# Optimization experiments

Measured on AMD Instinct MI355X. Metric: run time of the kernel, lower is better.

## Reference

```python
import jax, jax.numpy as jnp
import numpy as np
from jax import lax
from jax.scipy.special import logsumexp

XY, Z, V, WS = 16, 8, 10000, 2
S = XY * XY * Z            # 2048 states
EMB, TOK, HID = 256, 100, 256
B, T, L = 8, 16, 12
EPS = 1e-5


def residual(x, w1, b1, w2, b2, g, beta):
    # ResidualLayer: relu(lin1) -> relu(lin2) -> LayerNorm(x2 + x1)
    x1 = jax.nn.relu(x @ w1.T + b1)
    x2 = jax.nn.relu(x1 @ w2.T + b2)
    h = x2 + x1
    mu = h.mean(-1, keepdims=True)
    var = ((h - mu) ** 2).mean(-1, keepdims=True)
    return (h - mu) * lax.rsqrt(var + EPS) * g + beta


def win_logmean(m, axis, ws):
    win = 2 * ws + 1
    pads = [(0, 0)] * m.ndim
    pads[axis] = (ws, ws)
    p = jnp.pad(m, pads, mode='edge')
    d = m.shape[axis]
    acc = lax.dynamic_slice_in_dim(p, 0, d, axis)
    for k in range(1, win):
        acc = jnp.logaddexp(acc, lax.dynamic_slice_in_dim(p, k, d, axis))
    return acc - jnp.log(jnp.float32(win))


def setup_inputs() -> dict:
    key = jax.random.key(0)
    it = iter(jax.random.split(key, 64))

    def rn(shape, scale=0.05):
        return jax.random.normal(next(it), shape, jnp.float32) * scale

    inp = {}
    inp['state_emb'] = jax.random.normal(next(it), (S, EMB), jnp.float32)
    inp['tok_emb'] = jax.random.normal(next(it), (V, TOK), jnp.float32)

    def res(pfx, din, dout):
        inp[pfx + '_w1'] = rn((dout, din))
        inp[pfx + '_b1'] = jnp.zeros((dout,), jnp.float32)
        inp[pfx + '_w2'] = rn((dout, dout))
        inp[pfx + '_b2'] = jnp.zeros((dout,), jnp.float32)
        inp[pfx + '_g'] = jnp.ones((dout,), jnp.float32)
        inp[pfx + '_beta'] = jnp.zeros((dout,), jnp.float32)

    res('start', EMB, HID)
    inp['start_wo'] = rn((1, HID))
    inp['start_bo'] = jnp.zeros((1,), jnp.float32)
    res('tin', EMB, HID)
    res('tout', EMB, HID)
    res('emit', EMB, TOK)
    inp['stories'] = jax.random.randint(next(it), (B, T, L), 0, V + 1)  # id V = pad
    inp['story_length'] = T
    return inp


def reference(state_emb, tok_emb,
              start_w1, start_b1, start_w2, start_b2, start_g, start_beta, start_wo, start_bo,
              tin_w1, tin_b1, tin_w2, tin_b2, tin_g, tin_beta,
              tout_w1, tout_b1, tout_w2, tout_b2, tout_g, tout_beta,
              emit_w1, emit_b1, emit_w2, emit_b2, emit_g, emit_beta,
              stories, story_length):
    # prior_log_p: [S]
    h0 = residual(state_emb, start_w1, start_b1, start_w2, start_b2, start_g, start_beta)
    priors = jax.nn.log_softmax((h0 @ start_wo.T + start_bo)[:, 0], axis=-1)

    # transition_log_p: sparse-neighbor masked [S,S] log-softmax
    h_in = residual(state_emb, tin_w1, tin_b1, tin_w2, tin_b2, tin_g, tin_beta)
    h_out = residual(state_emb, tout_w1, tout_b1, tout_w2, tout_b2, tout_g, tout_beta)
    trans = h_in @ h_out.T
    idx = jnp.arange(S)
    offs = jnp.array([0, 1, -1, XY, -XY, XY * XY, 2 * XY * XY])
    neigh = idx[:, None] + offs[None, :]                        # [S,7]
    allowed = (neigh[:, :, None] == idx[None, None, :]).any(1)  # allowed[j,i]
    trans = jax.nn.log_softmax(jnp.where(allowed, trans, -jnp.inf), axis=-1)

    # emission matrix with windowed log-mean pooling over x,y
    h_emit = residual(state_emb, emit_w1, emit_b1, emit_w2, emit_b2, emit_g, emit_beta)
    em = jax.nn.log_softmax(h_emit @ tok_emb.T, axis=1)         # [S,V]
    em = em.reshape(Z, XY, XY, V)
    em = win_logmean(em, 2, WS)   # dim -2
    em = win_logmean(em, 1, WS)   # dim -3
    em = em.reshape(S, V)
    em_pad = jnp.concatenate([em, jnp.zeros((S, 1), em.dtype)], axis=1)  # pad token
    emis = em_pad.T[stories].sum(2)                             # [B,T,S]

    # HMM forward recursion in log domain
    score0 = emis[:, 0] + priors[None, :]

    def step(score, em_t):
        new = em_t + logsumexp(trans[None, :, :] + score[:, None, :], axis=-1)
        return new, new

    _, rest = lax.scan(step, score0, jnp.moveaxis(emis[:, 1:story_length], 1, 0))
    return jnp.concatenate([score0[None], rest], axis=0)        # [T,B,S]
```

## Files before the change

kernel.cpp:

```cpp
#include <hip/hip_runtime.h>
#include <hip/hip_bf16.h>
#include <math.h>


typedef __bf16 bf16_t;
typedef __bf16 bf16x8 __attribute__((ext_vector_type(8)));
typedef float  floatx4 __attribute__((ext_vector_type(4)));
typedef short  short8  __attribute__((ext_vector_type(8)));

#define S_TOT 2048
#define NT2 79
#define LSE_LD 80
#define VPAD 10112

__global__ __launch_bounds__(256) void tokconv_k(const float* __restrict__ src,
                                                 bf16_t* __restrict__ dst) {
    int idx = blockIdx.x * 256 + threadIdx.x;
    int r = idx >> 7, c = idx & 127;
    float v = (r < 10000 && c < 100) ? src[r * 100 + c] : 0.f;
    dst[idx] = (bf16_t)v;
}

struct GJob {
    const float*  Af;
    const bf16_t* Ab;
    int lda;
    const float* B; int ldb;
    int N, Nrows, K, Kvalid;
    float* C; int ldc;
    const float* bias; int nbias;
    const float* addm; int ldadd;
    bf16_t* Cbf; int ldcb;
};
struct GJobs { GJob j[4]; };

#define BM 64
#define BN 64
#define LDT 72

template<int EPI, int A32>
__global__ __launch_bounds__(256) void gemm_k(GJobs jobs) {
    GJob jb = jobs.j[blockIdx.z];
    const int m0 = blockIdx.x * BM;
    const int n0 = blockIdx.y * BN;
    if (n0 >= jb.N) return;

    __shared__ alignas(16) bf16_t As[BM * LDT];
    __shared__ alignas(16) bf16_t Bs[BN * LDT];
    const int tid  = threadIdx.x;
    const int lane = tid & 63, wave = tid >> 6;
    const int wm = (wave & 1) * 32, wn = (wave >> 1) * 32;
    const int sr = tid >> 2, scc = (tid & 3) * 16;
    const int qm = lane & 15, qk = (lane >> 4) * 8;

    floatx4 acc[2][2];
    floatx4 zf = {0.f, 0.f, 0.f, 0.f};
#pragma unroll
    for (int i = 0; i < 2; i++)
#pragma unroll
        for (int j = 0; j < 2; j++) acc[i][j] = zf;

    const bool brv = (n0 + sr) < jb.Nrows;

    for (int k0 = 0; k0 < jb.K; k0 += 64) {
        if constexpr (A32) {
            const float* Ar = jb.Af + (size_t)(m0 + sr) * jb.lda + k0 + scc;
            alignas(16) bf16_t ta[16];
#pragma unroll
            for (int i = 0; i < 4; i++) {
                float4 f = ((const float4*)Ar)[i];
                ta[i * 4 + 0] = (bf16_t)f.x; ta[i * 4 + 1] = (bf16_t)f.y;
                ta[i * 4 + 2] = (bf16_t)f.z; ta[i * 4 + 3] = (bf16_t)f.w;
            }
            *(short8*)&As[sr * LDT + scc]     = *(short8*)&ta[0];
            *(short8*)&As[sr * LDT + scc + 8] = *(short8*)&ta[8];
        } else {
            const bf16_t* Ar = jb.Ab + (size_t)(m0 + sr) * jb.lda + k0 + scc;
            *(short8*)&As[sr * LDT + scc]     = *(const short8*)&Ar[0];
            *(short8*)&As[sr * LDT + scc + 8] = *(const short8*)&Ar[8];
        }
        {
            const float* Br = jb.B + (size_t)(n0 + sr) * jb.ldb + k0 + scc;
            alignas(16) bf16_t tb[16];
#pragma unroll
            for (int i = 0; i < 4; i++) {
                int c4 = k0 + scc + i * 4;
                float4 f = {0.f, 0.f, 0.f, 0.f};
                if (brv && c4 < jb.Kvalid) f = *(const float4*)&Br[i * 4];
                tb[i * 4 + 0] = (bf16_t)f.x; tb[i * 4 + 1] = (bf16_t)f.y;
                tb[i * 4 + 2] = (bf16_t)f.z; tb[i * 4 + 3] = (bf16_t)f.w;
            }
            *(short8*)&Bs[sr * LDT + scc]     = *(short8*)&tb[0];
            *(short8*)&Bs[sr * LDT + scc + 8] = *(short8*)&tb[8];
        }
        __syncthreads();
#pragma unroll
        for (int kk = 0; kk < 2; kk++) {
            int qo = kk * 32 + qk;
            bf16x8 a[2], b[2];
            a[0] = *(const bf16x8*)&As[(wm + qm) * LDT + qo];
            a[1] = *(const bf16x8*)&As[(wm + 16 + qm) * LDT + qo];
            b[0] = *(const bf16x8*)&Bs[(wn + qm) * LDT + qo];
            b[1] = *(const bf16x8*)&Bs[(wn + 16 + qm) * LDT + qo];
#pragma unroll
            for (int mi = 0; mi < 2; mi++)
#pragma unroll
                for (int ni = 0; ni < 2; ni++)
                    acc[mi][ni] = __builtin_amdgcn_mfma_f32_16x16x32_bf16(a[mi], b[ni], acc[mi][ni], 0, 0, 0);
        }
        __syncthreads();
    }

    const int cl = lane & 15, rq = (lane >> 4) * 4;
#pragma unroll
    for (int mi = 0; mi < 2; mi++)
#pragma unroll
        for (int ni = 0; ni < 2; ni++)
#pragma unroll
            for (int r = 0; r < 4; r++) {
                int gm = m0 + wm + mi * 16 + rq + r;
                int gn = n0 + wn + ni * 16 + cl;
                if (gn < jb.N) {
                    float bv = (gn < jb.nbias) ? jb.bias[gn] : 0.f;
                    float v = fmaxf(acc[mi][ni][r] + bv, 0.f);
                    if constexpr (EPI == 1) {
                        jb.C[(size_t)gm * jb.ldc + gn] = v;
                        jb.Cbf[(size_t)gm * jb.ldcb + gn] = (bf16_t)v;
                    } else {
                        jb.C[(size_t)gm * jb.ldc + gn] = v + jb.addm[(size_t)gm * jb.ldadd + gn];
                    }
                }
            }
}

struct LJob {
    const float* h; int ld, dout;
    const float* g; const float* beta;
    float* of32; int ldo;
    bf16_t* obf; int ldob; int padN;
    const float* wo; const float* bo; float* praw;
};
struct LJobs { LJob j[4]; };

__global__ __launch_bounds__(256) void ln_k(LJobs jobs) {
    LJob jb = jobs.j[blockIdx.y];
    __shared__ float red[256];
    int row = blockIdx.x, t = threadIdx.x;
    float hv = (t < jb.dout) ? jb.h[(size_t)row * jb.ld + t] : 0.f;
    red[t] = hv;
    __syncthreads();
#pragma unroll
    for (int s = 128; s > 0; s >>= 1) { if (t < s) red[t] += red[t + s]; __syncthreads(); }
    float mu = red[0] / jb.dout;
    __syncthreads();
    float d = (t < jb.dout) ? (hv - mu) : 0.f;
    red[t] = d * d;
    __syncthreads();
#pragma unroll
    for (int s = 128; s > 0; s >>= 1) { if (t < s) red[t] += red[t + s]; __syncthreads(); }
    float var = red[0] / jb.dout;
    float rstd = rsqrtf(var + 1e-5f);
    float y = 0.f;
    if (t < jb.dout) {
        y = d * rstd * jb.g[t] + jb.beta[t];
        if (jb.of32) jb.of32[(size_t)row * jb.ldo + t] = y;
        if (jb.obf)  jb.obf[(size_t)row * jb.ldob + t] = (bf16_t)y;
    } else if (jb.obf && t < jb.padN) {
        jb.obf[(size_t)row * jb.ldob + t] = (bf16_t)0.f;
    }
    if (jb.wo) {
        __syncthreads();
        red[t] = (t < jb.dout) ? y * jb.wo[t] : 0.f;
        __syncthreads();
#pragma unroll
        for (int s = 128; s > 0; s >>= 1) { if (t < s) red[t] += red[t + s]; __syncthreads(); }
        if (t == 0) jb.praw[row] = red[0] + jb.bo[0];
    }
}

__global__ __launch_bounds__(256) void trans_k(const float* __restrict__ hin,
                                               const float* __restrict__ hout,
                                               float* __restrict__ tr,
                                               const float* __restrict__ praw,
                                               float* __restrict__ plse)
{
    __shared__ float red[256];
    if (blockIdx.x == 512) {
        int t = threadIdx.x;
        float v[8];
        float m = -INFINITY;
#pragma unroll
        for (int i = 0; i < 8; i++) { v[i] = praw[t * 8 + i]; m = fmaxf(m, v[i]); }
        red[t] = m;
        __syncthreads();
#pragma unroll
        for (int s = 128; s > 0; s >>= 1) { if (t < s) red[t] = fmaxf(red[t], red[t + s]); __syncthreads(); }
        float M = red[0];
        __syncthreads();
        float ss = 0.f;
#pragma unroll
        for (int i = 0; i < 8; i++) ss += __expf(v[i] - M);
        red[t] = ss;
        __syncthreads();
#pragma unroll
        for (int s = 128; s > 0; s >>= 1) { if (t < s) red[t] += red[t + s]; __syncthreads(); }
        if (t == 0) plse[0] = M + __logf(red[0]);
        return;
    }
    const int OFFS[7] = {0, 1, -1, 16, -16, 256, 512};
    int j = blockIdx.x * 4 + (threadIdx.x >> 6);
    int lane = threadIdx.x & 63;
    float4 a = ((const float4*)(hin + (size_t)j * 256))[lane];
    float d[7];
#pragma unroll
    for (int k = 0; k < 7; k++) {
        int i = j + OFFS[k];
        float pdot = 0.f;
        if ((unsigned)i < 2048u) {
            float4 b = ((const float4*)(hout + (size_t)i * 256))[lane];
            pdot = a.x * b.x + a.y * b.y + a.z * b.z + a.w * b.w;
        }
#pragma unroll
        for (int o = 32; o > 0; o >>= 1) pdot += __shfl_down(pdot, o);
        d[k] = pdot;
    }
    if (lane == 0) {
        float m = -INFINITY;
#pragma unroll
        for (int k = 0; k < 7; k++) { int i = j + OFFS[k]; if ((unsigned)i < 2048u) m = fmaxf(m, d[k]); }
        float ss = 0.f;
#pragma unroll
        for (int k = 0; k < 7; k++) { int i = j + OFFS[k]; if ((unsigned)i < 2048u) ss += __expf(d[k] - m); }
        float l = __logf(ss);
#pragma unroll
        for (int k = 0; k < 7; k++) {
            int i = j + OFFS[k];
            tr[(size_t)j * 8 + k] = ((unsigned)i < 2048u) ? (d[k] - m - l) : -INFINITY;
        }
        tr[(size_t)j * 8 + 7] = -INFINITY;
    }
}

__global__ __launch_bounds__(256) void lse_gemm_k(
    const bf16_t* __restrict__ hemit, const bf16_t* __restrict__ tok_bf,
    float* __restrict__ Pmax, float* __restrict__ Psum)
{
    __shared__ float pmS[2][128];
    __shared__ float psS[2][128];
    const int mb = blockIdx.x * 128;
    const int n0 = blockIdx.y * 128;
    const int tid  = threadIdx.x;
    const int lane = tid & 63, wave = tid >> 6;
    const int wm = (wave & 1) * 64, wn = (wave >> 1) * 64;
    const int qm = lane & 15, q = lane >> 4;

    floatx4 acc[4][4];
    floatx4 zf = {0.f, 0.f, 0.f, 0.f};
#pragma unroll
    for (int i = 0; i < 4; i++)
#pragma unroll
        for (int j = 0; j < 4; j++) acc[i][j] = zf;

    const bf16_t* Aw = hemit  + (size_t)(mb + wm + qm) * 128 + q * 8;
    const bf16_t* Bw = tok_bf + (size_t)(n0 + wn + qm) * 128 + q * 8;

#pragma unroll
    for (int kk = 0; kk < 4; kk++) {
        bf16x8 a[4], b[4];
#pragma unroll
        for (int i = 0; i < 4; i++) a[i] = *(const bf16x8*)&Aw[(size_t)(i * 16) * 128 + kk * 32];
#pragma unroll
        for (int i = 0; i < 4; i++) b[i] = *(const bf16x8*)&Bw[(size_t)(i * 16) * 128 + kk * 32];
#pragma unroll
        for (int mi = 0; mi < 4; mi++)
#pragma unroll
            for (int ni = 0; ni < 4; ni++)
                acc[mi][ni] = __builtin_amdgcn_mfma_f32_16x16x32_bf16(a[mi], b[ni], acc[mi][ni], 0, 0, 0);
    }

    const int cl = lane & 15, rq = (lane >> 4) * 4;
    const int half = wn >> 6;
#pragma unroll
    for (int mi = 0; mi < 4; mi++) {
#pragma unroll
        for (int r = 0; r < 4; r++) {
            float mm = -INFINITY;
#pragma unroll
            for (int ni = 0; ni < 4; ni++) {
                int gcol = n0 + wn + ni * 16 + cl;
                if (gcol < 10000) mm = fmaxf(mm, acc[mi][ni][r]);
            }
            mm = fmaxf(mm, __shfl_xor(mm, 1));
            mm = fmaxf(mm, __shfl_xor(mm, 2));
            mm = fmaxf(mm, __shfl_xor(mm, 4));
            mm = fmaxf(mm, __shfl_xor(mm, 8));
            float ss = 0.f;
#pragma unroll
            for (int ni = 0; ni < 4; ni++) {
                int gcol = n0 + wn + ni * 16 + cl;
                if (gcol < 10000) ss += __expf(acc[mi][ni][r] - mm);
            }
            ss += __shfl_xor(ss, 1);
            ss += __shfl_xor(ss, 2);
            ss += __shfl_xor(ss, 4);
            ss += __shfl_xor(ss, 8);
            if (cl == 0) {
                int row = wm + mi * 16 + rq + r;
                pmS[half][row] = mm;
                psS[half][row] = ss;
            }
        }
    }
    __syncthreads();
    if (tid < 128) {
        float ma = pmS[0][tid], mb2 = pmS[1][tid];
        float M = fmaxf(ma, mb2);
        float S = psS[0][tid] * __expf(ma - M) + psS[1][tid] * __expf(mb2 - M);
        Pmax[(size_t)(mb + tid) * LSE_LD + blockIdx.y] = M;
        Psum[(size_t)(mb + tid) * LSE_LD + blockIdx.y] = S;
    }
}

__global__ __launch_bounds__(256) void lse_fin_k(const float* __restrict__ Pmax,
                                                 const float* __restrict__ Psum,
                                                 float* __restrict__ lse)
{
    int s = (blockIdx.x * 256 + threadIdx.x) >> 6;
    int lane = threadIdx.x & 63;
    const float* pm = Pmax + (size_t)s * LSE_LD;
    const float* ps = Psum + (size_t)s * LSE_LD;
    float pv[2], sv[2];
    float m = -INFINITY;
#pragma unroll
    for (int i = 0; i < 2; i++) {
        int nb = i * 64 + lane;
        bool ok = nb < NT2;
        pv[i] = ok ? pm[nb] : -INFINITY;
        sv[i] = ok ? ps[nb] : 0.f;
        m = fmaxf(m, pv[i]);
    }
#pragma unroll
    for (int o = 1; o < 64; o <<= 1) m = fmaxf(m, __shfl_xor(m, o));
    float ss = 0.f;
#pragma unroll
    for (int i = 0; i < 2; i++) if (sv[i] > 0.f) ss += sv[i] * __expf(pv[i] - m);
#pragma unroll
    for (int o = 1; o < 64; o <<= 1) ss += __shfl_xor(ss, o);
    if (lane == 0) lse[s] = m + __logf(ss);
}

#define ELDT 136
__global__ __launch_bounds__(256) void empool_k(
    const float* __restrict__ tok_emb, const int* __restrict__ stories,
    const bf16_t* __restrict__ hemit, const float* __restrict__ lse,
    float* __restrict__ emis)
{
    __shared__ alignas(16) bf16_t As[16 * ELDT];
    __shared__ float Cs[16][260];
    __shared__ float sm2[256];
    __shared__ int stok[12];
    const int bt = blockIdx.x, z = blockIdx.y, t = threadIdx.x;
    if (t < 12) stok[t] = stories[bt * 12 + t];
    __syncthreads();
    {
        int row = t >> 4, c0 = (t & 15) * 8;
        int tok = (row < 12) ? stok[row] : 10000;
        const float* src = tok_emb + (size_t)tok * 100;
#pragma unroll
        for (int c = 0; c < 8; c++) {
            int cc = c0 + c;
            float v = (tok < 10000 && cc < 100) ? src[cc] : 0.f;
            As[row * ELDT + cc] = (bf16_t)v;
        }
    }
    __syncthreads();

    const int lane = t & 63, wave = t >> 6;
    const int qm = lane & 15, q = lane >> 4;
    floatx4 acc[4];
    floatx4 zf = {0.f, 0.f, 0.f, 0.f};
#pragma unroll
    for (int j = 0; j < 4; j++) acc[j] = zf;

#pragma unroll
    for (int kk = 0; kk < 4; kk++) {
        bf16x8 a = *(const bf16x8*)&As[qm * ELDT + kk * 32 + q * 8];
#pragma unroll
        for (int j = 0; j < 4; j++) {
            int nrow = z * 256 + (wave * 4 + j) * 16 + qm;
            bf16x8 b = *(const bf16x8*)&hemit[(size_t)nrow * 128 + kk * 32 + q * 8];
            acc[j] = __builtin_amdgcn_mfma_f32_16x16x32_bf16(a, b, acc[j], 0, 0, 0);
        }
    }
    {
        const int cl = lane & 15, rq = (lane >> 4) * 4;
#pragma unroll
        for (int j = 0; j < 4; j++) {
            int n = (wave * 4 + j) * 16 + cl;
            float ls = lse[z * 256 + n];
#pragma unroll
            for (int r = 0; r < 4; r++)
                Cs[rq + r][n] = acc[j][r] - ls;
        }
    }
    __syncthreads();

    const int a = t >> 4, b = t & 15;
    float accum = 0.f;
    for (int l = 0; l < 12; l++) {
        float m = -INFINITY;
#pragma unroll
        for (int d = -2; d <= 2; d++) {
            int bb = b + d; bb = bb < 0 ? 0 : (bb > 15 ? 15 : bb);
            m = fmaxf(m, Cs[l][a * 16 + bb]);
        }
        float ss = 0.f;
#pragma unroll
        for (int d = -2; d <= 2; d++) {
            int bb = b + d; bb = bb < 0 ? 0 : (bb > 15 ? 15 : bb);
            ss += __expf(Cs[l][a * 16 + bb] - m);
        }
        sm2[t] = m + __logf(ss);
        __syncthreads();
        float m2 = -INFINITY;
#pragma unroll
        for (int d = -2; d <= 2; d++) {
            int aa = a + d; aa = aa < 0 ? 0 : (aa > 15 ? 15 : aa);
            m2 = fmaxf(m2, sm2[aa * 16 + b]);
        }
        float s2 = 0.f;
#pragma unroll
        for (int d = -2; d <= 2; d++) {
            int aa = a + d; aa = aa < 0 ? 0 : (aa > 15 ? 15 : aa);
            s2 += __expf(sm2[aa * 16 + b] - m2);
        }
        if (stok[l] < 10000) accum += m2 + __logf(s2) - 3.2188758248682006f;
        __syncthreads();
    }
    emis[(size_t)bt * S_TOT + (size_t)z * 256 + t] = accum;
}

__global__ __launch_bounds__(1024) void fwd_k(const float* __restrict__ emm,
                                              const float* __restrict__ praw,
                                              const float* __restrict__ plse,
                                              const float* __restrict__ tr,
                                              float* __restrict__ out)
{
    const int OFFS[7] = {0, 1, -1, 16, -16, 256, 512};
    __shared__ float sc[2][S_TOT];
    int b = blockIdx.x, t = threadIdx.x;
    float pl = plse[0];
    const float* eb = emm + (size_t)b * 16 * S_TOT;

    float e[2][16];
#pragma unroll
    for (int i = 0; i < 2; i++) {
        int j = i * 1024 + t;
#pragma unroll
        for (int tt = 0; tt < 16; tt++) e[i][tt] = eb[tt * S_TOT + j];
    }
    float trj[2][7];
#pragma unroll
    for (int i = 0; i < 2; i++) {
        int j = i * 1024 + t;
        float4 lo = ((const float4*)(tr + (size_t)j * 8))[0];
        float4 hi = ((const float4*)(tr + (size_t)j * 8))[1];
        trj[i][0] = lo.x; trj[i][1] = lo.y; trj[i][2] = lo.z; trj[i][3] = lo.w;
        trj[i][4] = hi.x; trj[i][5] = hi.y; trj[i][6] = hi.z;
    }
#pragma unroll
    for (int i = 0; i < 2; i++) {
        int j = i * 1024 + t;
        float v = e[i][0] + praw[j] - pl;
        sc[0][j] = v;
        out[(size_t)b * S_TOT + j] = v;
    }
    __syncthreads();
#pragma unroll
    for (int tt = 1; tt < 16; tt++) {
        int cur = tt & 1, prv = cur ^ 1;
#pragma unroll
        for (int i = 0; i < 2; i++) {
            int j = i * 1024 + t;
            float x[7];
            float m = -INFINITY;
#pragma unroll
            for (int k = 0; k < 7; k++) {
                int ii = j + OFFS[k];
                ii = ii < 0 ? 0 : (ii > 2047 ? 2047 : ii);
                x[k] = trj[i][k] + sc[prv][ii];
                m = fmaxf(m, x[k]);
            }
            float ss = 0.f;
#pragma unroll
            for (int k = 0; k < 7; k++) ss += __expf(x[k] - m);
            float v = e[i][tt] + m + __logf(ss);
            sc[cur][j] = v;
            out[(size_t)tt * (8 * S_TOT) + (size_t)b * S_TOT + j] = v;
        }
        __syncthreads();
    }
}

extern "C" void kernel_launch(void* const* d_in, const int* in_sizes, int n_in,
                              void* d_out, int out_size, void* d_ws, size_t ws_size,
                              hipStream_t stream)
{
    (void)in_sizes; (void)n_in; (void)out_size; (void)ws_size;
    const float* state_emb  = (const float*)d_in[0];
    const float* tok_emb    = (const float*)d_in[1];
    const float* start_w1   = (const float*)d_in[2];
    const float* start_b1   = (const float*)d_in[3];
    const float* start_w2   = (const float*)d_in[4];
    const float* start_b2   = (const float*)d_in[5];
    const float* start_g    = (const float*)d_in[6];
    const float* start_beta = (const float*)d_in[7];
    const float* start_wo   = (const float*)d_in[8];
    const float* start_bo   = (const float*)d_in[9];
    const float* tin_w1     = (const float*)d_in[10];
    const float* tin_b1     = (const float*)d_in[11];
    const float* tin_w2     = (const float*)d_in[12];
    const float* tin_b2     = (const float*)d_in[13];
    const float* tin_g      = (const float*)d_in[14];
    const float* tin_beta   = (const float*)d_in[15];
    const float* tout_w1    = (const float*)d_in[16];
    const float* tout_b1    = (const float*)d_in[17];
    const float* tout_w2    = (const float*)d_in[18];
    const float* tout_b2    = (const float*)d_in[19];
    const float* tout_g     = (const float*)d_in[20];
    const float* tout_beta  = (const float*)d_in[21];
    const float* emit_w1    = (const float*)d_in[22];
    const float* emit_b1    = (const float*)d_in[23];
    const float* emit_w2    = (const float*)d_in[24];
    const float* emit_b2    = (const float*)d_in[25];
    const float* emit_g     = (const float*)d_in[26];
    const float* emit_beta  = (const float*)d_in[27];
    const int*   stories    = (const int*)d_in[28];
    float* out = (float*)d_out;

    char* base = (char*)d_ws;
    size_t off = 0;
    auto carve = [&](size_t bytes) -> char* {
        char* r = base + off;
        off = (off + bytes + 255) & ~(size_t)255;
        return r;
    };

    bf16_t* hemit  = (bf16_t*)carve((size_t)2048 * 128 * 2);
    bf16_t* tok_bf = (bf16_t*)carve((size_t)VPAD * 128 * 2);
    float*  hin    = (float*)carve((size_t)2048 * 256 * 4);
    float*  hout   = (float*)carve((size_t)2048 * 256 * 4);
    float*  praw   = (float*)carve((size_t)2048 * 4);
    float*  plse   = (float*)carve(256);
    float*  trans  = (float*)carve((size_t)2048 * 8 * 4);
    float*  pmax   = (float*)carve((size_t)2048 * LSE_LD * 4);
    float*  psum   = (float*)carve((size_t)2048 * LSE_LD * 4);
    float*  lse    = (float*)carve((size_t)2048 * 4);
    float*  emis   = (float*)carve((size_t)128 * 2048 * 4);

    float*  x1f_s  = (float*)carve((size_t)2048 * 256 * 4);
    float*  x1f_i  = (float*)carve((size_t)2048 * 256 * 4);
    float*  x1f_o  = (float*)carve((size_t)2048 * 256 * 4);
    float*  x1f_e  = (float*)carve((size_t)2048 * 128 * 4);
    bf16_t* x1b_s  = (bf16_t*)carve((size_t)2048 * 256 * 2);
    bf16_t* x1b_i  = (bf16_t*)carve((size_t)2048 * 256 * 2);
    bf16_t* x1b_o  = (bf16_t*)carve((size_t)2048 * 256 * 2);
    bf16_t* x1b_e  = (bf16_t*)carve((size_t)2048 * 128 * 2);
    float*  htmp_s = (float*)carve((size_t)2048 * 256 * 4);
    float*  htmp_i = (float*)carve((size_t)2048 * 256 * 4);
    float*  htmp_o = (float*)carve((size_t)2048 * 256 * 4);
    float*  htmp_e = (float*)carve((size_t)2048 * 128 * 4);

    tokconv_k<<<(VPAD * 128) / 256, 256, 0, stream>>>(tok_emb, tok_bf);

    GJobs g1;
    g1.j[0] = {state_emb, nullptr, 256, start_w1, 256, 256, 256, 256, 256, x1f_s, 256, start_b1, 256, nullptr, 0, x1b_s, 256};
    g1.j[1] = {state_emb, nullptr, 256, tin_w1,   256, 256, 256, 256, 256, x1f_i, 256, tin_b1,   256, nullptr, 0, x1b_i, 256};
    g1.j[2] = {state_emb, nullptr, 256, tout_w1,  256, 256, 256, 256, 256, x1f_o, 256, tout_b1,  256, nullptr, 0, x1b_o, 256};
    g1.j[3] = {state_emb, nullptr, 256, emit_w1,  256, 128, 100, 256, 256, x1f_e, 128, emit_b1,  100, nullptr, 0, x1b_e, 128};
    gemm_k<1, 1><<<dim3(32, 4, 4), 256, 0, stream>>>(g1);

    GJobs g2;
    g2.j[0] = {nullptr, x1b_s, 256, start_w2, 256, 256, 256, 256, 256, htmp_s, 256, start_b2, 256, x1f_s, 256, nullptr, 0};
    g2.j[1] = {nullptr, x1b_i, 256, tin_w2,   256, 256, 256, 256, 256, htmp_i, 256, tin_b2,   256, x1f_i, 256, nullptr, 0};
    g2.j[2] = {nullptr, x1b_o, 256, tout_w2,  256, 256, 256, 256, 256, htmp_o, 256, tout_b2,  256, x1f_o, 256, nullptr, 0};
    g2.j[3] = {nullptr, x1b_e, 128, emit_w2,  100, 128, 100, 128, 100, htmp_e, 128, emit_b2,  100, x1f_e, 128, nullptr, 0};
    gemm_k<2, 0><<<dim3(32, 4, 4), 256, 0, stream>>>(g2);

    LJobs lj;
    lj.j[0] = {htmp_s, 256, 256, start_g, start_beta, nullptr, 0, nullptr, 0, 0, start_wo, start_bo, praw};
    lj.j[1] = {htmp_i, 256, 256, tin_g,   tin_beta,   hin, 256, nullptr, 0, 0, nullptr, nullptr, nullptr};
    lj.j[2] = {htmp_o, 256, 256, tout_g,  tout_beta,  hout, 256, nullptr, 0, 0, nullptr, nullptr, nullptr};
    lj.j[3] = {htmp_e, 128, 100, emit_g,  emit_beta,  nullptr, 0, hemit, 128, 128, nullptr, nullptr, nullptr};
    ln_k<<<dim3(2048, 4), 256, 0, stream>>>(lj);

    trans_k<<<513, 256, 0, stream>>>(hin, hout, trans, praw, plse);

    lse_gemm_k<<<dim3(16, NT2), 256, 0, stream>>>(hemit, tok_bf, pmax, psum);
    lse_fin_k<<<512, 256, 0, stream>>>(pmax, psum, lse);

    empool_k<<<dim3(128, 8), 256, 0, stream>>>(tok_emb, stories, hemit, lse, emis);

    fwd_k<<<8, 1024, 0, stream>>>(emis, praw, plse, trans, out);
}
```

Before: 220.3 us.

## Fuse residual layer GEMMs and LayerNorm into one kernel with bf16 prepacked weights

Replaces the two batched GEMM launches and the separate LayerNorm launch with a single kernel per 32-row block. It computes lin1, relu, lin2, relu, the residual add and LayerNorm entirely in shared memory, reading weights pre-converted to zero-padded bf16. A generalized prep kernel converts the token embedding and all eight weight matrices in one launch. This removes intermediate global round-trips and launch overhead. In exchange, the x1 residual term is now taken from its bf16 copy rather than fp32, and weights are read straight from global memory without LDS staging.

New measurement: 227.4 us. 3.2% more time.

```diff
diff --git a/kernel.cpp b/kernel.cpp
--- a/kernel.cpp
+++ b/kernel.cpp
@@ -13,168 +13,142 @@
 #define LSE_LD 80
 #define VPAD 10112
 
-__global__ __launch_bounds__(256) void tokconv_k(const float* __restrict__ src,
-                                                 bf16_t* __restrict__ dst) {
-    int idx = blockIdx.x * 256 + threadIdx.x;
-    int r = idx >> 7, c = idx & 127;
-    float v = (r < 10000 && c < 100) ? src[r * 100 + c] : 0.f;
-    dst[idx] = (bf16_t)v;
-}
-
-struct GJob {
-    const float*  Af;
-    const bf16_t* Ab;
-    int lda;
-    const float* B; int ldb;
-    int N, Nrows, K, Kvalid;
-    float* C; int ldc;
-    const float* bias; int nbias;
-    const float* addm; int ldadd;
-    bf16_t* Cbf; int ldcb;
-};
-struct GJobs { GJob j[4]; };
-
-#define BM 64
-#define BN 64
-#define LDT 72
-
-template<int EPI, int A32>
-__global__ __launch_bounds__(256) void gemm_k(GJobs jobs) {
-    GJob jb = jobs.j[blockIdx.z];
-    const int m0 = blockIdx.x * BM;
-    const int n0 = blockIdx.y * BN;
-    if (n0 >= jb.N) return;
-
-    __shared__ alignas(16) bf16_t As[BM * LDT];
-    __shared__ alignas(16) bf16_t Bs[BN * LDT];
-    const int tid  = threadIdx.x;
-    const int lane = tid & 63, wave = tid >> 6;
-    const int wm = (wave & 1) * 32, wn = (wave >> 1) * 32;
-    const int sr = tid >> 2, scc = (tid & 3) * 16;
-    const int qm = lane & 15, qk = (lane >> 4) * 8;
-
-    floatx4 acc[2][2];
-    floatx4 zf = {0.f, 0.f, 0.f, 0.f};
-#pragma unroll
-    for (int i = 0; i < 2; i++)
-#pragma unroll
-        for (int j = 0; j < 2; j++) acc[i][j] = zf;
-
-    const bool brv = (n0 + sr) < jb.Nrows;
-
-    for (int k0 = 0; k0 < jb.K; k0 += 64) {
-        if constexpr (A32) {
-            const float* Ar = jb.Af + (size_t)(m0 + sr) * jb.lda + k0 + scc;
-            alignas(16) bf16_t ta[16];
-#pragma unroll
-            for (int i = 0; i < 4; i++) {
-                float4 f = ((const float4*)Ar)[i];
-                ta[i * 4 + 0] = (bf16_t)f.x; ta[i * 4 + 1] = (bf16_t)f.y;
-                ta[i * 4 + 2] = (bf16_t)f.z; ta[i * 4 + 3] = (bf16_t)f.w;
-            }
-            *(short8*)&As[sr * LDT + scc]     = *(short8*)&ta[0];
-            *(short8*)&As[sr * LDT + scc + 8] = *(short8*)&ta[8];
-        } else {
-            const bf16_t* Ar = jb.Ab + (size_t)(m0 + sr) * jb.lda + k0 + scc;
-            *(short8*)&As[sr * LDT + scc]     = *(const short8*)&Ar[0];
-            *(short8*)&As[sr * LDT + scc + 8] = *(const short8*)&Ar[8];
-        }
-        {
-            const float* Br = jb.B + (size_t)(n0 + sr) * jb.ldb + k0 + scc;
-            alignas(16) bf16_t tb[16];
-#pragma unroll
-            for (int i = 0; i < 4; i++) {
-                int c4 = k0 + scc + i * 4;
-                float4 f = {0.f, 0.f, 0.f, 0.f};
-                if (brv && c4 < jb.Kvalid) f = *(const float4*)&Br[i * 4];
-                tb[i * 4 + 0] = (bf16_t)f.x; tb[i * 4 + 1] = (bf16_t)f.y;
-                tb[i * 4 + 2] = (bf16_t)f.z; tb[i * 4 + 3] = (bf16_t)f.w;
-            }
-            *(short8*)&Bs[sr * LDT + scc]     = *(short8*)&tb[0];
-            *(short8*)&Bs[sr * LDT + scc + 8] = *(short8*)&tb[8];
-        }
-        __syncthreads();
-#pragma unroll
-        for (int kk = 0; kk < 2; kk++) {
-            int qo = kk * 32 + qk;
-            bf16x8 a[2], b[2];
-            a[0] = *(const bf16x8*)&As[(wm + qm) * LDT + qo];
-            a[1] = *(const bf16x8*)&As[(wm + 16 + qm) * LDT + qo];
-            b[0] = *(const bf16x8*)&Bs[(wn + qm) * LDT + qo];
-            b[1] = *(const bf16x8*)&Bs[(wn + 16 + qm) * LDT + qo];
-#pragma unroll
-            for (int mi = 0; mi < 2; mi++)
-#pragma unroll
-                for (int ni = 0; ni < 2; ni++)
-                    acc[mi][ni] = __builtin_amdgcn_mfma_f32_16x16x32_bf16(a[mi], b[ni], acc[mi][ni], 0, 0, 0);
-        }
-        __syncthreads();
-    }
-
-    const int cl = lane & 15, rq = (lane >> 4) * 4;
-#pragma unroll
-    for (int mi = 0; mi < 2; mi++)
-#pragma unroll
-        for (int ni = 0; ni < 2; ni++)
-#pragma unroll
-            for (int r = 0; r < 4; r++) {
-                int gm = m0 + wm + mi * 16 + rq + r;
-                int gn = n0 + wn + ni * 16 + cl;
-                if (gn < jb.N) {
-                    float bv = (gn < jb.nbias) ? jb.bias[gn] : 0.f;
-                    float v = fmaxf(acc[mi][ni][r] + bv, 0.f);
-                    if constexpr (EPI == 1) {
-                        jb.C[(size_t)gm * jb.ldc + gn] = v;
-                        jb.Cbf[(size_t)gm * jb.ldcb + gn] = (bf16_t)v;
-                    } else {
-                        jb.C[(size_t)gm * jb.ldc + gn] = v + jb.addm[(size_t)gm * jb.ldadd + gn];
-                    }
-                }
-            }
-}
-
-struct LJob {
-    const float* h; int ld, dout;
-    const float* g; const float* beta;
-    float* of32; int ldo;
-    bf16_t* obf; int ldob; int padN;
+struct CJob { const float* src; bf16_t* dst; int srows, scols, drows, dcols; };
+struct CJobs { CJob j[9]; };
+
+__global__ __launch_bounds__(256) void prep_k(CJobs jobs) {
+    CJob job = jobs.j[blockIdx.y];
+    int total = job.drows * job.dcols;
+    for (int idx = blockIdx.x * 256 + threadIdx.x; idx < total; idx += gridDim.x * 256) {
+        int r = idx / job.dcols;
+        int c = idx - r * job.dcols;
+        float v = (r < job.srows && c < job.scols) ? job.src[(size_t)r * job.scols + c] : 0.f;
+        job.dst[idx] = (bf16_t)v;
+    }
+}
+
+struct RChain {
+    const bf16_t* W1; const bf16_t* W2;
+    const float* b1; int nb1;
+    const float* b2; int nb2;
+    const float* g; const float* beta; int dout;
+    float* ohf;
+    bf16_t* ohb;
     const float* wo; const float* bo; float* praw;
 };
-struct LJobs { LJob j[4]; };
-
-__global__ __launch_bounds__(256) void ln_k(LJobs jobs) {
-    LJob jb = jobs.j[blockIdx.y];
-    __shared__ float red[256];
-    int row = blockIdx.x, t = threadIdx.x;
-    float hv = (t < jb.dout) ? jb.h[(size_t)row * jb.ld + t] : 0.f;
-    red[t] = hv;
-    __syncthreads();
-#pragma unroll
-    for (int s = 128; s > 0; s >>= 1) { if (t < s) red[t] += red[t + s]; __syncthreads(); }
-    float mu = red[0] / jb.dout;
-    __syncthreads();
-    float d = (t < jb.dout) ? (hv - mu) : 0.f;
-    red[t] = d * d;
-    __syncthreads();
-#pragma unroll
-    for (int s = 128; s > 0; s >>= 1) { if (t < s) red[t] += red[t + s]; __syncthreads(); }
-    float var = red[0] / jb.dout;
-    float rstd = rsqrtf(var + 1e-5f);
-    float y = 0.f;
-    if (t < jb.dout) {
-        y = d * rstd * jb.g[t] + jb.beta[t];
-        if (jb.of32) jb.of32[(size_t)row * jb.ldo + t] = y;
-        if (jb.obf)  jb.obf[(size_t)row * jb.ldob + t] = (bf16_t)y;
-    } else if (jb.obf && t < jb.padN) {
-        jb.obf[(size_t)row * jb.ldob + t] = (bf16_t)0.f;
-    }
-    if (jb.wo) {
-        __syncthreads();
-        red[t] = (t < jb.dout) ? y * jb.wo[t] : 0.f;
-        __syncthreads();
-#pragma unroll
-        for (int s = 128; s > 0; s >>= 1) { if (t < s) red[t] += red[t + s]; __syncthreads(); }
-        if (t == 0) jb.praw[row] = red[0] + jb.bo[0];
+struct RChains { RChain j[4]; };
+
+#define RLD 264
+
+__global__ __launch_bounds__(256) void resid_k(const float* __restrict__ se, RChains ch) {
+    RChain c = ch.j[blockIdx.y];
+    const int m0 = blockIdx.x * 32;
+    __shared__ char smem[33792 + 16896];
+    bf16_t* As = (bf16_t*)smem;
+    float*  Hs = (float*)smem;
+    bf16_t* Xs = (bf16_t*)(smem + 33792);
+
+    const int tid  = threadIdx.x;
+    const int lane = tid & 63, w = tid >> 6;
+    const int cl = lane & 15, q = lane >> 4;
+    const int rowg = (w & 1) * 16;
+    const int nh   = (w >> 1) * 128;
+
+    {
+        int sr = tid >> 3, cb = (tid & 7) * 32;
+        const float4* src = (const float4*)(se + (size_t)(m0 + sr) * 256 + cb);
+#pragma unroll
+        for (int i = 0; i < 4; i++) {
+            float4 f0 = src[i * 2], f1 = src[i * 2 + 1];
+            alignas(16) bf16_t tmp[8] = {(bf16_t)f0.x, (bf16_t)f0.y, (bf16_t)f0.z, (bf16_t)f0.w,
+                                         (bf16_t)f1.x, (bf16_t)f1.y, (bf16_t)f1.z, (bf16_t)f1.w};
+            *(short8*)&As[sr * RLD + cb + i * 8] = *(short8*)tmp;
+        }
+    }
+    __syncthreads();
+
+    floatx4 acc[8];
+    floatx4 zf = {0.f, 0.f, 0.f, 0.f};
+#pragma unroll
+    for (int i = 0; i < 8; i++) acc[i] = zf;
+
+#pragma unroll
+    for (int kk = 0; kk < 8; kk++) {
+        bf16x8 a = *(const bf16x8*)&As[(rowg + cl) * RLD + kk * 32 + q * 8];
+#pragma unroll
+        for (int ni = 0; ni < 8; ni++) {
+            bf16x8 b = *(const bf16x8*)&c.W1[(size_t)(nh + ni * 16 + cl) * 256 + kk * 32 + q * 8];
+            acc[ni] = __builtin_amdgcn_mfma_f32_16x16x32_bf16(a, b, acc[ni], 0, 0, 0);
+        }
+    }
+#pragma unroll
+    for (int ni = 0; ni < 8; ni++)
+#pragma unroll
+        for (int r = 0; r < 4; r++) {
+            int n = nh + ni * 16 + cl;
+            int lr = rowg + q * 4 + r;
+            float v = acc[ni][r] + (n < c.nb1 ? c.b1[n] : 0.f);
+            Xs[lr * RLD + n] = (bf16_t)fmaxf(v, 0.f);
+        }
+    __syncthreads();
+
+#pragma unroll
+    for (int i = 0; i < 8; i++) acc[i] = zf;
+#pragma unroll
+    for (int kk = 0; kk < 8; kk++) {
+        bf16x8 a = *(const bf16x8*)&Xs[(rowg + cl) * RLD + kk * 32 + q * 8];
+#pragma unroll
+        for (int ni = 0; ni < 8; ni++) {
+            bf16x8 b = *(const bf16x8*)&c.W2[(size_t)(nh + ni * 16 + cl) * 256 + kk * 32 + q * 8];
+            acc[ni] = __builtin_amdgcn_mfma_f32_16x16x32_bf16(a, b, acc[ni], 0, 0, 0);
+        }
+    }
+#pragma unroll
+    for (int ni = 0; ni < 8; ni++)
+#pragma unroll
+        for (int r = 0; r < 4; r++) {
+            int n = nh + ni * 16 + cl;
+            int lr = rowg + q * 4 + r;
+            float v = fmaxf(acc[ni][r] + (n < c.nb2 ? c.b2[n] : 0.f), 0.f);
+            Hs[lr * 264 + n] = v + (float)Xs[lr * RLD + n];
+        }
+    __syncthreads();
+
+    {
+        int row = tid >> 3, c0 = (tid & 7) * 32;
+        float s1 = 0.f, s2 = 0.f;
+#pragma unroll
+        for (int i = 0; i < 32; i++) {
+            int cc = c0 + i;
+            if (cc < c.dout) { float h = Hs[row * 264 + cc]; s1 += h; s2 += h * h; }
+        }
+        s1 += __shfl_xor(s1, 1); s2 += __shfl_xor(s2, 1);
+        s1 += __shfl_xor(s1, 2); s2 += __shfl_xor(s2, 2);
+        s1 += __shfl_xor(s1, 4); s2 += __shfl_xor(s2, 4);
+        float inv = 1.f / (float)c.dout;
+        float mu = s1 * inv;
+        float var = s2 * inv - mu * mu;
+        float rstd = rsqrtf(var + 1e-5f);
+        int gm = m0 + row;
+        float pr = 0.f;
+#pragma unroll
+        for (int i = 0; i < 32; i++) {
+            int cc = c0 + i;
+            if (cc < c.dout) {
+                float y = (Hs[row * 264 + cc] - mu) * rstd * c.g[cc] + c.beta[cc];
+                if (c.ohf) c.ohf[(size_t)gm * 256 + cc] = y;
+                if (c.ohb) c.ohb[(size_t)gm * 128 + cc] = (bf16_t)y;
+                if (c.wo)  pr += y * c.wo[cc];
+            } else if (c.ohb && cc < 128) {
+                c.ohb[(size_t)gm * 128 + cc] = (bf16_t)0.f;
+            }
+        }
+        if (c.wo) {
+            pr += __shfl_xor(pr, 1);
+            pr += __shfl_xor(pr, 2);
+            pr += __shfl_xor(pr, 4);
+            if ((tid & 7) == 0) c.praw[gm] = pr + c.bo[0];
+        }
     }
 }
 
@@ -548,6 +522,7 @@
 
     bf16_t* hemit  = (bf16_t*)carve((size_t)2048 * 128 * 2);
     bf16_t* tok_bf = (bf16_t*)carve((size_t)VPAD * 128 * 2);
+    bf16_t* wpad   = (bf16_t*)carve((size_t)8 * 256 * 256 * 2);
     float*  hin    = (float*)carve((size_t)2048 * 256 * 4);
     float*  hout   = (float*)carve((size_t)2048 * 256 * 4);
     float*  praw   = (float*)carve((size_t)2048 * 4);
@@ -558,41 +533,37 @@
     float*  lse    = (float*)carve((size_t)2048 * 4);
     float*  emis   = (float*)carve((size_t)128 * 2048 * 4);
 
-    float*  x1f_s  = (float*)carve((size_t)2048 * 256 * 4);
-    float*  x1f_i  = (float*)carve((size_t)2048 * 256 * 4);
-    float*  x1f_o  = (float*)carve((size_t)2048 * 256 * 4);
-    float*  x1f_e  = (float*)carve((size_t)2048 * 128 * 4);
-    bf16_t* x1b_s  = (bf16_t*)carve((size_t)2048 * 256 * 2);
-    bf16_t* x1b_i  = (bf16_t*)carve((size_t)2048 * 256 * 2);
-    bf16_t* x1b_o  = (bf16_t*)carve((size_t)2048 * 256 * 2);
-    bf16_t* x1b_e  = (bf16_t*)carve((size_t)2048 * 128 * 2);
-    float*  htmp_s = (float*)carve((size_t)2048 * 256 * 4);
-    float*  htmp_i = (float*)carve((size_t)2048 * 256 * 4);
-    float*  htmp_o = (float*)carve((size_t)2048 * 256 * 4);
-    float*  htmp_e = (float*)carve((size_t)2048 * 128 * 4);
-
-    tokconv_k<<<(VPAD * 128) / 256, 256, 0, stream>>>(tok_emb, tok_bf);
-
-    GJobs g1;
-    g1.j[0] = {state_emb, nullptr, 256, start_w1, 256, 256, 256, 256, 256, x1f_s, 256, start_b1, 256, nullptr, 0, x1b_s, 256};
-    g1.j[1] = {state_emb, nullptr, 256, tin_w1,   256, 256, 256, 256, 256, x1f_i, 256, tin_b1,   256, nullptr, 0, x1b_i, 256};
-    g1.j[2] = {state_emb, nullptr, 256, tout_w1,  256, 256, 256, 256, 256, x1f_o, 256, tout_b1,  256, nullptr, 0, x1b_o, 256};
-    g1.j[3] = {state_emb, nullptr, 256, emit_w1,  256, 128, 100, 256, 256, x1f_e, 128, emit_b1,  100, nullptr, 0, x1b_e, 128};
-    gemm_k<1, 1><<<dim3(32, 4, 4), 256, 0, stream>>>(g1);
-
-    GJobs g2;
-    g2.j[0] = {nullptr, x1b_s, 256, start_w2, 256, 256, 256, 256, 256, htmp_s, 256, start_b2, 256, x1f_s, 256, nullptr, 0};
-    g2.j[1] = {nullptr, x1b_i, 256, tin_w2,   256, 256, 256, 256, 256, htmp_i, 256, tin_b2,   256, x1f_i, 256, nullptr, 0};
-    g2.j[2] = {nullptr, x1b_o, 256, tout_w2,  256, 256, 256, 256, 256, htmp_o, 256, tout_b2,  256, x1f_o, 256, nullptr, 0};
-    g2.j[3] = {nullptr, x1b_e, 128, emit_w2,  100, 128, 100, 128, 100, htmp_e, 128, emit_b2,  100, x1f_e, 128, nullptr, 0};
-    gemm_k<2, 0><<<dim3(32, 4, 4), 256, 0, stream>>>(g2);
-
-    LJobs lj;
-    lj.j[0] = {htmp_s, 256, 256, start_g, start_beta, nullptr, 0, nullptr, 0, 0, start_wo, start_bo, praw};
-    lj.j[1] = {htmp_i, 256, 256, tin_g,   tin_beta,   hin, 256, nullptr, 0, 0, nullptr, nullptr, nullptr};
-    lj.j[2] = {htmp_o, 256, 256, tout_g,  tout_beta,  hout, 256, nullptr, 0, 0, nullptr, nullptr, nullptr};
-    lj.j[3] = {htmp_e, 128, 100, emit_g,  emit_beta,  nullptr, 0, hemit, 128, 128, nullptr, nullptr, nullptr};
-    ln_k<<<dim3(2048, 4), 256, 0, stream>>>(lj);
+    bf16_t* w_s1 = wpad + 0 * 65536;
+    bf16_t* w_s2 = wpad + 1 * 65536;
+    bf16_t* w_i1 = wpad + 2 * 65536;
+    bf16_t* w_i2 = wpad + 3 * 65536;
+    bf16_t* w_o1 = wpad + 4 * 65536;
+    bf16_t* w_o2 = wpad + 5 * 65536;
+    bf16_t* w_e1 = wpad + 6 * 65536;
+    bf16_t* w_e2 = wpad + 7 * 65536;
+
+    CJobs cj;
+    cj.j[0] = {tok_emb,  tok_bf, 10000, 100, VPAD, 128};
+    cj.j[1] = {start_w1, w_s1, 256, 256, 256, 256};
+    cj.j[2] = {start_w2, w_s2, 256, 256, 256, 256};
+    cj.j[3] = {tin_w1,   w_i1, 256, 256, 256, 256};
+    cj.j[4] = {tin_w2,   w_i2, 256, 256, 256, 256};
+    cj.j[5] = {tout_w1,  w_o1, 256, 256, 256, 256};
+    cj.j[6] = {tout_w2,  w_o2, 256, 256, 256, 256};
+    cj.j[7] = {emit_w1,  w_e1, 100, 256, 256, 256};
+    cj.j[8] = {emit_w2,  w_e2, 100, 100, 256, 256};
+    prep_k<<<dim3(512, 9), 256, 0, stream>>>(cj);
+
+    RChains rc;
+    rc.j[0] = {w_s1, w_s2, start_b1, 256, start_b2, 256, start_g, start_beta, 256,
+               nullptr, nullptr, start_wo, start_bo, praw};
+    rc.j[1] = {w_i1, w_i2, tin_b1, 256, tin_b2, 256, tin_g, tin_beta, 256,
+               hin, nullptr, nullptr, nullptr, nullptr};
+    rc.j[2] = {w_o1, w_o2, tout_b1, 256, tout_b2, 256, tout_g, tout_beta, 256,
+               hout, nullptr, nullptr, nullptr, nullptr};
+    rc.j[3] = {w_e1, w_e2, emit_b1, 100, emit_b2, 100, emit_g, emit_beta, 100,
+               nullptr, hemit, nullptr, nullptr, nullptr};
+    resid_k<<<dim3(64, 4), 256, 0, stream>>>(state_emb, rc);
 
     trans_k<<<513, 256, 0, stream>>>(hin, hout, trans, praw, plse);
 
```
